# Optimization experiments

Hardware: AMD Instinct MI355X
Metric: run time of the kernel (lower is better)

Reference implementation:

```python
import jax, jax.numpy as jnp
import numpy as np

B, N, DIN, DOUT = 16384, 32, 128, 256
ITERS = 3
SQUASH_W = 1.0
EPS_SQUASH = 1e-9
EPS_NORM = 1e-12


def setup_inputs() -> dict:
    key = jax.random.key(0)
    k1, k2, k3 = jax.random.split(key, 3)
    embeds = jax.random.normal(k1, (B, N, DIN), dtype=jnp.float32)
    weights = jax.random.normal(k2, (B, N), dtype=jnp.float32)
    # xavier_normal init for Linear weight, zero-ish bias (torch default bias is
    # uniform but value is irrelevant for a correctness baseline; keep it small)
    xav = float(np.sqrt(2.0 / (DIN + DOUT)))
    W = jax.random.normal(k3, (DIN, DOUT), dtype=jnp.float32) * xav
    b = jnp.zeros((DOUT,), dtype=jnp.float32)
    return {"embeds": embeds, "weights": weights, "W": W, "b": b}


def _squash(s):
    # s: [B, D]; squash along the capsule vector dim D (axis=-2 in the original
    # [B,1,1,D,1] layout == last axis here).
    sq = jnp.sum(s * s, axis=-1, keepdims=True)
    scale = sq / (SQUASH_W + sq) / jnp.sqrt(sq + EPS_SQUASH)
    return scale * s


def reference(embeds, weights, W, b):
    # Linear + (eval-mode) dropout identity; no activation (default None)
    x = jnp.einsum("bni,io->bno", embeds, W) + b          # [B, N, DOUT]
    # F.normalize(p=2, dim=-2) over the capsule vector dim
    nrm = jnp.sqrt(jnp.sum(x * x, axis=-1, keepdims=True))
    u_hat = x / jnp.maximum(nrm, EPS_NORM)                 # [B, N, DOUT]
    u_hat_det = jax.lax.stop_gradient(u_hat)

    b_ij = weights[:, :, None]                             # [B, N, 1]
    c_ij = None
    v = None
    for r in range(ITERS):
        c_ij = jax.nn.softmax(b_ij, axis=1) * N            # [B, N, 1]
        s = jnp.sum(c_ij * u_hat, axis=1)                  # [B, DOUT]
        v = _squash(s)                                     # [B, DOUT]
        if r < ITERS - 1:
            # u_hat^T v  -> per-candidate agreement scalar
            agree = jnp.einsum("bnd,bd->bn", u_hat_det, v)
            b_ij = b_ij + agree[:, :, None]
    poses = v                                              # [B, DOUT]
    c_out = c_ij[:, :, 0]                                  # [B, N]
    return (poses, c_out)
```

## Files before the change

### kernel.cpp

```cpp
#include <hip/hip_runtime.h>
#include <hip/hip_bf16.h>

typedef __attribute__((ext_vector_type(8))) __bf16 bf16x8;
typedef __attribute__((ext_vector_type(4))) __bf16 bf16x4;
typedef __attribute__((ext_vector_type(4))) float  f32x4;

#define B_    16384
#define N_    32
#define DIN_  128
#define DOUT_ 256

__global__ void prep_w(const float* __restrict__ W, __bf16* __restrict__ wp) {
    int tid = blockIdx.x * 256 + threadIdx.x;
    int ks = tid >> 10;
    int ot = (tid >> 6) & 15;
    int l  = tid & 63;
    int k0 = ks * 32 + ((l >> 4) << 3);
    int o  = ot * 16 + (l & 15);
    __bf16 v[8];
#pragma unroll
    for (int j = 0; j < 8; ++j) v[j] = (__bf16)W[(size_t)(k0 + j) * DOUT_ + o];
    *reinterpret_cast<bf16x8*>(&wp[(size_t)tid * 8]) = *reinterpret_cast<bf16x8*>(v);
}

__global__ __launch_bounds__(256, 4) void dyr_main(
    const float* __restrict__ embeds, const float* __restrict__ weights,
    const __bf16* __restrict__ wp,    const float* __restrict__ bias,
    float* __restrict__ out)
{
    __shared__ __bf16 elds[32 * 136];
    __shared__ float  red[4][32];
    __shared__ float  agl[4 * 32];
    __shared__ float  bsh[32];
    __shared__ float  rn[32];
    __shared__ float  sqp[4];

    const int tid = threadIdx.x;
    const int w   = tid >> 6;
    const int l   = tid & 63;
    const int col = l & 15;
    const int q   = l >> 4;
    const int b   = blockIdx.x;

    const float4* e4 = reinterpret_cast<const float4*>(embeds + (size_t)b * N_ * DIN_);
#pragma unroll
    for (int p = 0; p < 4; ++p) {
        int fi = p * 256 + tid;
        float4 v = e4[fi];
        int m = fi >> 5;
        int k = (fi & 31) << 2;
        __bf16 pk[4] = { (__bf16)v.x, (__bf16)v.y, (__bf16)v.z, (__bf16)v.w };
        *reinterpret_cast<bf16x4*>(&elds[m * 136 + k]) = *reinterpret_cast<bf16x4*>(pk);
    }
    if (tid < 32) bsh[tid] = weights[(size_t)b * N_ + tid];
    __syncthreads();

    f32x4 acc[2][4];
#pragma unroll
    for (int mt = 0; mt < 2; ++mt)
#pragma unroll
        for (int t = 0; t < 4; ++t) acc[mt][t] = (f32x4){0.f, 0.f, 0.f, 0.f};

    const int aoff0 = col * 136 + (q << 3);
#pragma unroll
    for (int ks = 0; ks < 4; ++ks) {
        bf16x8 a0 = *reinterpret_cast<const bf16x8*>(&elds[aoff0 + ks * 32]);
        bf16x8 a1 = *reinterpret_cast<const bf16x8*>(&elds[aoff0 + 16 * 136 + ks * 32]);
#pragma unroll
        for (int t = 0; t < 4; ++t) {
            bf16x8 bf = *reinterpret_cast<const bf16x8*>(
                &wp[((size_t)((ks * 16) + (w * 4 + t)) * 64 + l) * 8]);
            acc[0][t] = __builtin_amdgcn_mfma_f32_16x16x32_bf16(a0, bf, acc[0][t], 0, 0, 0);
            acc[1][t] = __builtin_amdgcn_mfma_f32_16x16x32_bf16(a1, bf, acc[1][t], 0, 0, 0);
        }
    }

#pragma unroll
    for (int t = 0; t < 4; ++t) {
        float bv = bias[w * 64 + t * 16 + col];
#pragma unroll
        for (int mt = 0; mt < 2; ++mt)
#pragma unroll
            for (int r = 0; r < 4; ++r) acc[mt][t][r] += bv;
    }

#pragma unroll
    for (int mt = 0; mt < 2; ++mt)
#pragma unroll
        for (int r = 0; r < 4; ++r) {
            float p = 0.f;
#pragma unroll
            for (int t = 0; t < 4; ++t) p += acc[mt][t][r] * acc[mt][t][r];
            p += __shfl_xor(p, 1); p += __shfl_xor(p, 2);
            p += __shfl_xor(p, 4); p += __shfl_xor(p, 8);
            if (col == 0) red[w][mt * 16 + q * 4 + r] = p;
        }
    __syncthreads();
    if (tid < 32) {
        float nsq = red[0][tid] + red[1][tid] + red[2][tid] + red[3][tid];
        rn[tid] = 1.0f / fmaxf(sqrtf(nsq), 1e-12f);
    }
    __syncthreads();
#pragma unroll
    for (int mt = 0; mt < 2; ++mt)
#pragma unroll
        for (int r = 0; r < 4; ++r) {
            float s = rn[mt * 16 + q * 4 + r];
#pragma unroll
            for (int t = 0; t < 4; ++t) acc[mt][t][r] *= s;
        }

    float cme = 0.f;
    float vv[4] = {0.f, 0.f, 0.f, 0.f};
    for (int it = 0; it < 3; ++it) {
        float bval = bsh[l & 31];
        float mx = bval;
        mx = fmaxf(mx, __shfl_xor(mx, 16)); mx = fmaxf(mx, __shfl_xor(mx, 8));
        mx = fmaxf(mx, __shfl_xor(mx, 4));  mx = fmaxf(mx, __shfl_xor(mx, 2));
        mx = fmaxf(mx, __shfl_xor(mx, 1));
        float ex = __expf(bval - mx);
        float sm = ex;
        sm += __shfl_xor(sm, 16); sm += __shfl_xor(sm, 8); sm += __shfl_xor(sm, 4);
        sm += __shfl_xor(sm, 2);  sm += __shfl_xor(sm, 1);
        cme = ex * (32.0f / sm);

        float cv[2][4];
#pragma unroll
        for (int mt = 0; mt < 2; ++mt)
#pragma unroll
            for (int r = 0; r < 4; ++r) cv[mt][r] = __shfl(cme, mt * 16 + q * 4 + r);

        float sv[4];
#pragma unroll
        for (int t = 0; t < 4; ++t) {
            float s = 0.f;
#pragma unroll
            for (int mt = 0; mt < 2; ++mt)
#pragma unroll
                for (int r = 0; r < 4; ++r) s += cv[mt][r] * acc[mt][t][r];
            s += __shfl_xor(s, 16); s += __shfl_xor(s, 32);
            sv[t] = s;
        }

        float loc = sv[0]*sv[0] + sv[1]*sv[1] + sv[2]*sv[2] + sv[3]*sv[3];
        loc += __shfl_xor(loc, 1); loc += __shfl_xor(loc, 2);
        loc += __shfl_xor(loc, 4); loc += __shfl_xor(loc, 8);
        if (l == 0) sqp[w] = loc;
        __syncthreads();
        float sq = sqp[0] + sqp[1] + sqp[2] + sqp[3];
        float scale = sq / ((1.0f + sq) * sqrtf(sq + 1e-9f));
#pragma unroll
        for (int t = 0; t < 4; ++t) vv[t] = scale * sv[t];

        if (it < 2) {
#pragma unroll
            for (int mt = 0; mt < 2; ++mt)
#pragma unroll
                for (int r = 0; r < 4; ++r) {
                    float ap = 0.f;
#pragma unroll
                    for (int t = 0; t < 4; ++t) ap += acc[mt][t][r] * vv[t];
                    ap += __shfl_xor(ap, 1); ap += __shfl_xor(ap, 2);
                    ap += __shfl_xor(ap, 4); ap += __shfl_xor(ap, 8);
                    if (col == 0) agl[w * 32 + mt * 16 + q * 4 + r] = ap;
                }
            __syncthreads();
            if (tid < 32) bsh[tid] += agl[tid] + agl[32 + tid] + agl[64 + tid] + agl[96 + tid];
            __syncthreads();
        }
    }

    if (l < 16) {
#pragma unroll
        for (int t = 0; t < 4; ++t)
            out[(size_t)b * DOUT_ + w * 64 + t * 16 + l] = vv[t];
    }
    if (w == 0 && l < 32)
        out[(size_t)B_ * DOUT_ + (size_t)b * N_ + l] = cme;
}

extern "C" void kernel_launch(void* const* d_in, const int* in_sizes, int n_in,
                              void* d_out, int out_size, void* d_ws, size_t ws_size,
                              hipStream_t stream) {
    const float* embeds  = (const float*)d_in[0];
    const float* weights = (const float*)d_in[1];
    const float* W       = (const float*)d_in[2];
    const float* bias    = (const float*)d_in[3];
    float* out = (float*)d_out;
    __bf16* wp = (__bf16*)d_ws;

    prep_w<<<16, 256, 0, stream>>>(W, wp);
    dyr_main<<<B_, 256, 0, stream>>>(embeds, weights, wp, bias, out);
}
```

Baseline: 440.2 us.

## Map one batch row per wavefront, drop LDS and block barriers, use fp16 MFMA

Each wavefront now handles one whole batch element across all 256 output columns, with 16 output tiles per wave. Embeddings are loaded straight from global memory into MFMA operands, so LDS staging is gone, and every reduction (norm, squash, agreement) becomes a wave-local shuffle with no __syncthreads. The matmul switches from bf16 to fp16 MFMA inputs for better mantissa precision. In exchange each thread holds 128 accumulator floats, which is a lot of register pressure (launch bounds lowered to 1), so occupancy drops, and the global embed reads are strided per lane.

New measurement: 505.5 us. 1.15x slower.

```diff
diff --git a/kernel.cpp b/kernel.cpp
--- a/kernel.cpp
+++ b/kernel.cpp
@@ -1,87 +1,78 @@
 #include <hip/hip_runtime.h>
 #include <hip/hip_bf16.h>
 
-typedef __attribute__((ext_vector_type(8))) __bf16 bf16x8;
-typedef __attribute__((ext_vector_type(4))) __bf16 bf16x4;
-typedef __attribute__((ext_vector_type(4))) float  f32x4;
+typedef __attribute__((ext_vector_type(8))) _Float16 f16x8;
+typedef __attribute__((ext_vector_type(4))) float    f32x4;
 
 #define B_    16384
 #define N_    32
 #define DIN_  128
 #define DOUT_ 256
 
-__global__ void prep_w(const float* __restrict__ W, __bf16* __restrict__ wp) {
+__global__ void prep_w(const float* __restrict__ W, _Float16* __restrict__ wp) {
     int tid = blockIdx.x * 256 + threadIdx.x;
     int ks = tid >> 10;
     int ot = (tid >> 6) & 15;
     int l  = tid & 63;
     int k0 = ks * 32 + ((l >> 4) << 3);
     int o  = ot * 16 + (l & 15);
-    __bf16 v[8];
+    _Float16 v[8];
 #pragma unroll
-    for (int j = 0; j < 8; ++j) v[j] = (__bf16)W[(size_t)(k0 + j) * DOUT_ + o];
-    *reinterpret_cast<bf16x8*>(&wp[(size_t)tid * 8]) = *reinterpret_cast<bf16x8*>(v);
+    for (int j = 0; j < 8; ++j) v[j] = (_Float16)W[(size_t)(k0 + j) * DOUT_ + o];
+    *reinterpret_cast<f16x8*>(&wp[(size_t)tid * 8]) = *reinterpret_cast<f16x8*>(v);
 }
 
-__global__ __launch_bounds__(256, 4) void dyr_main(
+__global__ __launch_bounds__(256, 1) void dyr_main(
     const float* __restrict__ embeds, const float* __restrict__ weights,
-    const __bf16* __restrict__ wp,    const float* __restrict__ bias,
+    const _Float16* __restrict__ wp,  const float* __restrict__ bias,
     float* __restrict__ out)
 {
-    __shared__ __bf16 elds[32 * 136];
-    __shared__ float  red[4][32];
-    __shared__ float  agl[4 * 32];
-    __shared__ float  bsh[32];
-    __shared__ float  rn[32];
-    __shared__ float  sqp[4];
-
     const int tid = threadIdx.x;
-    const int w   = tid >> 6;
+    const int wv  = tid >> 6;
     const int l   = tid & 63;
     const int col = l & 15;
     const int q   = l >> 4;
-    const int b   = blockIdx.x;
+    const size_t b = (size_t)blockIdx.x * 4 + wv;
 
-    const float4* e4 = reinterpret_cast<const float4*>(embeds + (size_t)b * N_ * DIN_);
-#pragma unroll
-    for (int p = 0; p < 4; ++p) {
-        int fi = p * 256 + tid;
-        float4 v = e4[fi];
-        int m = fi >> 5;
-        int k = (fi & 31) << 2;
-        __bf16 pk[4] = { (__bf16)v.x, (__bf16)v.y, (__bf16)v.z, (__bf16)v.w };
-        *reinterpret_cast<bf16x4*>(&elds[m * 136 + k]) = *reinterpret_cast<bf16x4*>(pk);
-    }
-    if (tid < 32) bsh[tid] = weights[(size_t)b * N_ + tid];
-    __syncthreads();
+    const float* eb = embeds + b * (size_t)(N_ * DIN_);
 
-    f32x4 acc[2][4];
+    f32x4 acc[2][16];
 #pragma unroll
     for (int mt = 0; mt < 2; ++mt)
 #pragma unroll
-        for (int t = 0; t < 4; ++t) acc[mt][t] = (f32x4){0.f, 0.f, 0.f, 0.f};
+        for (int ot = 0; ot < 16; ++ot) acc[mt][ot] = (f32x4){0.f, 0.f, 0.f, 0.f};
 
-    const int aoff0 = col * 136 + (q << 3);
+    float bn = weights[b * N_ + (l & 31)];
+
 #pragma unroll
     for (int ks = 0; ks < 4; ++ks) {
-        bf16x8 a0 = *reinterpret_cast<const bf16x8*>(&elds[aoff0 + ks * 32]);
-        bf16x8 a1 = *reinterpret_cast<const bf16x8*>(&elds[aoff0 + 16 * 136 + ks * 32]);
+        f16x8 a[2];
 #pragma unroll
-        for (int t = 0; t < 4; ++t) {
-            bf16x8 bf = *reinterpret_cast<const bf16x8*>(
-                &wp[((size_t)((ks * 16) + (w * 4 + t)) * 64 + l) * 8]);
-            acc[0][t] = __builtin_amdgcn_mfma_f32_16x16x32_bf16(a0, bf, acc[0][t], 0, 0, 0);
-            acc[1][t] = __builtin_amdgcn_mfma_f32_16x16x32_bf16(a1, bf, acc[1][t], 0, 0, 0);
+        for (int mt = 0; mt < 2; ++mt) {
+            const float4* p4 = reinterpret_cast<const float4*>(
+                eb + (size_t)(mt * 16 + col) * DIN_ + ks * 32 + q * 8);
+            float4 r0 = p4[0];
+            float4 r1 = p4[1];
+            _Float16 av[8] = { (_Float16)r0.x, (_Float16)r0.y, (_Float16)r0.z, (_Float16)r0.w,
+                               (_Float16)r1.x, (_Float16)r1.y, (_Float16)r1.z, (_Float16)r1.w };
+            a[mt] = *reinterpret_cast<f16x8*>(av);
+        }
+#pragma unroll
+        for (int ot = 0; ot < 16; ++ot) {
+            f16x8 bf = *reinterpret_cast<const f16x8*>(
+                &wp[((size_t)(ks * 16 + ot) * 64 + l) * 8]);
+            acc[0][ot] = __builtin_amdgcn_mfma_f32_16x16x32_f16(a[0], bf, acc[0][ot], 0, 0, 0);
+            acc[1][ot] = __builtin_amdgcn_mfma_f32_16x16x32_f16(a[1], bf, acc[1][ot], 0, 0, 0);
         }
     }
 
 #pragma unroll
-    for (int t = 0; t < 4; ++t) {
-        float bv = bias[w * 64 + t * 16 + col];
+    for (int ot = 0; ot < 16; ++ot) {
+        float bv = bias[ot * 16 + col];
 #pragma unroll
         for (int mt = 0; mt < 2; ++mt)
 #pragma unroll
-            for (int r = 0; r < 4; ++r) acc[mt][t][r] += bv;
+            for (int r = 0; r < 4; ++r) acc[mt][ot][r] += bv;
     }
 
 #pragma unroll
@@ -90,38 +81,26 @@
         for (int r = 0; r < 4; ++r) {
             float p = 0.f;
 #pragma unroll
-            for (int t = 0; t < 4; ++t) p += acc[mt][t][r] * acc[mt][t][r];
+            for (int ot = 0; ot < 16; ++ot) p += acc[mt][ot][r] * acc[mt][ot][r];
             p += __shfl_xor(p, 1); p += __shfl_xor(p, 2);
             p += __shfl_xor(p, 4); p += __shfl_xor(p, 8);
-            if (col == 0) red[w][mt * 16 + q * 4 + r] = p;
-        }
-    __syncthreads();
-    if (tid < 32) {
-        float nsq = red[0][tid] + red[1][tid] + red[2][tid] + red[3][tid];
-        rn[tid] = 1.0f / fmaxf(sqrtf(nsq), 1e-12f);
-    }
-    __syncthreads();
+            float rn = 1.0f / fmaxf(sqrtf(p), 1e-12f);
 #pragma unroll
-    for (int mt = 0; mt < 2; ++mt)
-#pragma unroll
-        for (int r = 0; r < 4; ++r) {
-            float s = rn[mt * 16 + q * 4 + r];
-#pragma unroll
-            for (int t = 0; t < 4; ++t) acc[mt][t][r] *= s;
+            for (int ot = 0; ot < 16; ++ot) acc[mt][ot][r] *= rn;
         }
 
     float cme = 0.f;
-    float vv[4] = {0.f, 0.f, 0.f, 0.f};
+    float vv[16];
+#pragma unroll
     for (int it = 0; it < 3; ++it) {
-        float bval = bsh[l & 31];
-        float mx = bval;
-        mx = fmaxf(mx, __shfl_xor(mx, 16)); mx = fmaxf(mx, __shfl_xor(mx, 8));
-        mx = fmaxf(mx, __shfl_xor(mx, 4));  mx = fmaxf(mx, __shfl_xor(mx, 2));
-        mx = fmaxf(mx, __shfl_xor(mx, 1));
-        float ex = __expf(bval - mx);
+        float mx = bn;
+        mx = fmaxf(mx, __shfl_xor(mx, 1));  mx = fmaxf(mx, __shfl_xor(mx, 2));
+        mx = fmaxf(mx, __shfl_xor(mx, 4));  mx = fmaxf(mx, __shfl_xor(mx, 8));
+        mx = fmaxf(mx, __shfl_xor(mx, 16));
+        float ex = __expf(bn - mx);
         float sm = ex;
-        sm += __shfl_xor(sm, 16); sm += __shfl_xor(sm, 8); sm += __shfl_xor(sm, 4);
-        sm += __shfl_xor(sm, 2);  sm += __shfl_xor(sm, 1);
+        sm += __shfl_xor(sm, 1); sm += __shfl_xor(sm, 2); sm += __shfl_xor(sm, 4);
+        sm += __shfl_xor(sm, 8); sm += __shfl_xor(sm, 16);
         cme = ex * (32.0f / sm);
 
         float cv[2][4];
@@ -130,53 +109,67 @@
 #pragma unroll
             for (int r = 0; r < 4; ++r) cv[mt][r] = __shfl(cme, mt * 16 + q * 4 + r);
 
-        float sv[4];
+        float sv[16];
 #pragma unroll
-        for (int t = 0; t < 4; ++t) {
+        for (int ot = 0; ot < 16; ++ot) {
             float s = 0.f;
 #pragma unroll
             for (int mt = 0; mt < 2; ++mt)
 #pragma unroll
-                for (int r = 0; r < 4; ++r) s += cv[mt][r] * acc[mt][t][r];
+                for (int r = 0; r < 4; ++r) s += cv[mt][r] * acc[mt][ot][r];
             s += __shfl_xor(s, 16); s += __shfl_xor(s, 32);
-            sv[t] = s;
+            sv[ot] = s;
         }
 
-        float loc = sv[0]*sv[0] + sv[1]*sv[1] + sv[2]*sv[2] + sv[3]*sv[3];
-        loc += __shfl_xor(loc, 1); loc += __shfl_xor(loc, 2);
-        loc += __shfl_xor(loc, 4); loc += __shfl_xor(loc, 8);
-        if (l == 0) sqp[w] = loc;
-        __syncthreads();
-        float sq = sqp[0] + sqp[1] + sqp[2] + sqp[3];
+        float sq = 0.f;
+#pragma unroll
+        for (int ot = 0; ot < 16; ++ot) sq += sv[ot] * sv[ot];
+        sq += __shfl_xor(sq, 1); sq += __shfl_xor(sq, 2);
+        sq += __shfl_xor(sq, 4); sq += __shfl_xor(sq, 8);
         float scale = sq / ((1.0f + sq) * sqrtf(sq + 1e-9f));
 #pragma unroll
-        for (int t = 0; t < 4; ++t) vv[t] = scale * sv[t];
+        for (int ot = 0; ot < 16; ++ot) vv[ot] = scale * sv[ot];
 
         if (it < 2) {
+            float ag[2][4];
 #pragma unroll
             for (int mt = 0; mt < 2; ++mt)
 #pragma unroll
                 for (int r = 0; r < 4; ++r) {
                     float ap = 0.f;
 #pragma unroll
-                    for (int t = 0; t < 4; ++t) ap += acc[mt][t][r] * vv[t];
+                    for (int ot = 0; ot < 16; ++ot) ap += acc[mt][ot][r] * vv[ot];
                     ap += __shfl_xor(ap, 1); ap += __shfl_xor(ap, 2);
                     ap += __shfl_xor(ap, 4); ap += __shfl_xor(ap, 8);
-                    if (col == 0) agl[w * 32 + mt * 16 + q * 4 + r] = ap;
+                    ag[mt][r] = ap;
                 }
-            __syncthreads();
-            if (tid < 32) bsh[tid] += agl[tid] + agl[32 + tid] + agl[64 + tid] + agl[96 + tid];
-            __syncthreads();
+            {
+                int srcl = ((l >> 2) & 3) << 4;
+                float t0[4], t1[4];
+#pragma unroll
+                for (int r = 0; r < 4; ++r) {
+                    t0[r] = __shfl(ag[0][r], srcl);
+                    t1[r] = __shfl(ag[1][r], srcl);
+                }
+                float tm[4];
+#pragma unroll
+                for (int r = 0; r < 4; ++r) tm[r] = ((l >> 4) & 1) ? t1[r] : t0[r];
+                float g0 = (l & 1) ? tm[1] : tm[0];
+                float g1 = (l & 1) ? tm[3] : tm[2];
+                bn += (l & 2) ? g1 : g0;
+            }
         }
     }
 
-    if (l < 16) {
 #pragma unroll
-        for (int t = 0; t < 4; ++t)
-            out[(size_t)b * DOUT_ + w * 64 + t * 16 + l] = vv[t];
+    for (int j = 0; j < 4; ++j) {
+        float v0 = (q & 1) ? vv[4 + j]  : vv[j];
+        float v1 = (q & 1) ? vv[12 + j] : vv[8 + j];
+        float val = (q & 2) ? v1 : v0;
+        out[b * DOUT_ + (size_t)(q * 4 + j) * 16 + col] = val;
     }
-    if (w == 0 && l < 32)
-        out[(size_t)B_ * DOUT_ + (size_t)b * N_ + l] = cme;
+    if (l < 32)
+        out[(size_t)B_ * DOUT_ + b * N_ + l] = cme;
 }
 
 extern "C" void kernel_launch(void* const* d_in, const int* in_sizes, int n_in,
@@ -187,8 +180,8 @@
     const float* W       = (const float*)d_in[2];
     const float* bias    = (const float*)d_in[3];
     float* out = (float*)d_out;
-    __bf16* wp = (__bf16*)d_ws;
+    _Float16* wp = (_Float16*)d_ws;
 
     prep_w<<<16, 256, 0, stream>>>(W, wp);
-    dyr_main<<<B_, 256, 0, stream>>>(embeds, weights, wp, bias, out);
+    dyr_main<<<B_ / 4, 256, 0, stream>>>(embeds, weights, wp, bias, out);
 }
```
